# Optimization experiments

Hardware: AMD Instinct MI355X
Metric: run time of the kernel (lower is better)

The kernel has to match this reference:

```python
import jax, jax.numpy as jnp
import numpy as np

N = 50000
E = 800000
IN_C = 256
OUT_C = 128
HID = 2 * OUT_C  # 256


def setup_inputs() -> dict:
    key = jax.random.key(0)
    ks = jax.random.split(key, 8)
    def glorot(k, fan_in, fan_out):
        lim = (6.0 / (fan_in + fan_out)) ** 0.5
        return jax.random.uniform(k, (fan_in, fan_out), jnp.float32, -lim, lim)
    x = jax.random.normal(ks[0], (N, IN_C), dtype=jnp.float32)
    edge_index = jax.random.randint(ks[1], (2, E), 0, N, dtype=jnp.int64)
    return {
        "x": x,
        "edge_index": edge_index,
        "W1": glorot(ks[2], IN_C, HID),
        "b1": jnp.zeros((HID,), jnp.float32),
        "W_mu": glorot(ks[3], HID, OUT_C),
        "b_mu": jnp.zeros((OUT_C,), jnp.float32),
        "W_ls": glorot(ks[4], HID, OUT_C),
        "b_ls": jnp.zeros((OUT_C,), jnp.float32),
    }


def _gcn_norm(edge_index, n):
    # PyG GCNConv default: add self-loops, symmetric normalization D^-1/2 A D^-1/2
    loop = jnp.arange(n, dtype=edge_index.dtype)
    src = jnp.concatenate([edge_index[0], loop])  # [E+N]
    dst = jnp.concatenate([edge_index[1], loop])
    deg = jax.ops.segment_sum(jnp.ones_like(dst, dtype=jnp.float32), dst, num_segments=n)
    dinv = jnp.where(deg > 0, jax.lax.rsqrt(deg), 0.0)
    norm = dinv[src] * dinv[dst]  # [E+N]
    return src, dst, norm


def _gcn_conv(x, W, b, src, dst, norm, n):
    h = x @ W                                   # [N, F_out] transform first (F_out < F_in ok)
    msg = h[src] * norm[:, None]                # [E+N, F_out] gather + scale
    out = jax.ops.segment_sum(msg, dst, num_segments=n)  # scatter-add aggregate
    return out + b


def reference(x, edge_index, W1, b1, W_mu, b_mu, W_ls, b_ls):
    n = x.shape[0]
    src, dst, norm = _gcn_norm(edge_index, n)
    h = jax.nn.relu(_gcn_conv(x, W1, b1, src, dst, norm, n))
    mu = _gcn_conv(h, W_mu, b_mu, src, dst, norm, n)
    logstd = _gcn_conv(h, W_ls, b_ls, src, dst, norm, n)
    return (mu, logstd)
```

## Files before the change

kernel.cpp:

```cpp
#include <hip/hip_runtime.h>

#define NN 50000
#define EE 800000
#define NBIN 196
#define BINCAP 4608
#define NB_P1 391
#define NB_PA 6250
#define NB_PB 256

typedef _Float16 half8 __attribute__((ext_vector_type(8)));
typedef float f32x4 __attribute__((ext_vector_type(4)));
typedef unsigned short ushort8v __attribute__((ext_vector_type(8)));
typedef unsigned short ushort4v __attribute__((ext_vector_type(4)));

__device__ __forceinline__ unsigned short f2h(float f){
  _Float16 h = (_Float16)f; unsigned short u; __builtin_memcpy(&u, &h, 2); return u;
}
__device__ __forceinline__ float h2f(unsigned short u){
  _Float16 h; __builtin_memcpy(&h, &u, 2); return (float)h;
}
__device__ __forceinline__ void split2h(float v, unsigned short* p){
  _Float16 hi = (_Float16)v;
  _Float16 lo = (_Float16)(v - (float)hi);
  __builtin_memcpy(p, &hi, 2);
  __builtin_memcpy(p+1, &lo, 2);
}
__device__ __forceinline__ void gl2lds16(const unsigned short* g, unsigned short* l){
  __builtin_amdgcn_global_load_lds(
    (const __attribute__((address_space(1))) unsigned int*)g,
    (__attribute__((address_space(3))) unsigned int*)l, 16, 0, 0);
}

__device__ __forceinline__ int detect_m(const int* eidx, int* sh){
  int t = threadIdx.x;
  if (t < 64){
    int v = eidx[2*t + 1];
    unsigned long long nz = __ballot(v != 0);
    if (t == 0) *sh = (nz == 0ULL) ? 1 : 0;
  }
  __syncthreads();
  return *sh;
}

__global__ __launch_bounds__(512) void k_prep(const int* __restrict__ eidx,
    const float* __restrict__ X, const float* __restrict__ W1,
    const float* __restrict__ Wmu, const float* __restrict__ Wls,
    int* __restrict__ gcur, unsigned int* __restrict__ binbuf,
    unsigned short* __restrict__ Asp, unsigned short* __restrict__ Bt1,
    unsigned short* __restrict__ Bt2){
  int b = blockIdx.x;
  int tid = threadIdx.x;
  if (b < NB_P1){
    __shared__ int msh;
    __shared__ int hist[NBIN];
    __shared__ int base[NBIN];
    int m = detect_m(eidx, &msh);
    for (int k = tid; k < NBIN; k += 512) hist[k] = 0;
    __syncthreads();
    int sv[4], dl[4], cb[4], ofs[4];
    #pragma unroll
    for (int j = 0; j < 4; ++j){
      int e = b*2048 + j*512 + tid;
      cb[j] = -1;
      if (e < EE){
        sv[j] = m ? eidx[2*e]        : eidx[e];
        int d  = m ? eidx[2*(EE + e)] : eidx[EE + e];
        cb[j] = d >> 8; dl[j] = d & 255;
        ofs[j] = atomicAdd(&hist[cb[j]], 1);
      }
    }
    __syncthreads();
    for (int k = tid; k < NBIN; k += 512)
      base[k] = hist[k] ? atomicAdd(&gcur[k], hist[k]) : 0;
    __syncthreads();
    #pragma unroll
    for (int j = 0; j < 4; ++j){
      if (cb[j] >= 0){
        int p = base[cb[j]] + ofs[j];
        if (p < BINCAP)
          binbuf[(size_t)cb[j]*BINCAP + p] = (unsigned)sv[j] | ((unsigned)dl[j] << 16);
      }
    }
  } else if (b < NB_P1 + NB_PA){
    int gid = (b - NB_P1)*512 + tid;
    int r = gid >> 6, t = gid & 63;
    float4 v = *(const float4*)(X + (size_t)r*256 + t*4);
    __attribute__((aligned(16))) unsigned short sh[8];
    split2h(v.x, sh); split2h(v.y, sh+2); split2h(v.z, sh+4); split2h(v.w, sh+6);
    *(uint4*)(Asp + (size_t)r*512 + t*8) = *(const uint4*)(sh);
  } else {
    int gid = (b - NB_P1 - NB_PA)*512 + tid;
    int idx = gid & 65535;
    int n = idx & 255, k = idx >> 8;
    if (gid < 65536){
      unsigned short hq = f2h(W1[k*256 + n]);
      unsigned short* p = Bt1 + (size_t)n*512 + 2*k;
      p[0] = hq; p[1] = hq;
    } else {
      float w = (n < 128) ? Wmu[k*128 + n] : Wls[k*128 + (n - 128)];
      Bt2[(size_t)n*256 + k] = f2h(w);
    }
  }
}

__global__ __launch_bounds__(512) void k_pass2(const unsigned int* __restrict__ binbuf,
    const int* __restrict__ gcur, int* __restrict__ cnt,
    unsigned short* __restrict__ bk){
  __shared__ int lcnt[256];
  __shared__ __align__(16) unsigned short lbk[256*64];
  int c = blockIdx.x;
  int tid = threadIdx.x;
  if (tid < 256) lcnt[tid] = 0;
  __syncthreads();
  int n = gcur[c]; if (n > BINCAP) n = BINCAP;
  const unsigned int* bb = binbuf + (size_t)c*BINCAP;
  for (int t = tid; t < n; t += 512){
    unsigned v = bb[t];
    int dloc = v >> 16;
    int slot = atomicAdd(&lcnt[dloc], 1);
    if (slot < 64) lbk[dloc*64 + slot] = (unsigned short)(v & 0xFFFF);
  }
  __syncthreads();
  #pragma unroll
  for (int k = 0; k < 4; ++k){
    int idx = k*512 + tid;
    int node = c*256 + (idx >> 3);
    if (node < NN)
      *(uint4*)(bk + (size_t)c*256*64 + idx*8) = *(const uint4*)(lbk + idx*8);
  }
  if (tid < 256){
    int node = c*256 + tid;
    if (node < NN) cnt[node] = lcnt[tid];
  }
}

template<int KT, int SCALE>
__global__ __launch_bounds__(256) void k_gemm(const unsigned short* __restrict__ Asp,
                                              const unsigned short* __restrict__ Bt,
                                              unsigned short* __restrict__ C, int M,
                                              const int* __restrict__ cnt){
  __shared__ __align__(16) unsigned short sA[128*64];
  __shared__ __align__(16) unsigned short sB[128*64];
  const int tid  = threadIdx.x;
  const int wave = tid >> 6, lane = tid & 63;
  const int wm = wave >> 1, wn = wave & 1;
  const int quad = lane >> 4, l16 = lane & 15;
  const int tM = blockIdx.x, tN = blockIdx.y;
  const int rsub = lane >> 3;
  const int chs  = (lane & 7) ^ rsub;

  f32x4 acc[4][4] = {};

  for (int kt = 0; kt < KT; ++kt){
    #pragma unroll
    for (int j = 0; j < 4; ++j){
      int q = wave*4 + j;
      int r = q*8 + rsub;
      int arow = tM*128 + r; if (arow >= M) arow = M-1;
      gl2lds16(Asp + (size_t)arow*(KT*64) + kt*64 + chs*8, &sA[q*512]);
      gl2lds16(Bt  + (size_t)(tN*128 + r)*(KT*64) + kt*64 + chs*8, &sB[q*512]);
    }
    __syncthreads();
    #pragma unroll
    for (int ks = 0; ks < 2; ++ks){
      half8 af[4], bfr[4];
      #pragma unroll
      for (int t = 0; t < 4; ++t){
        int R = wm*64 + t*16 + l16;
        af[t]  = *(const half8*)(&sA[R*64 + ((ks*4 + quad) ^ (R & 7))*8]);
      }
      #pragma unroll
      for (int t = 0; t < 4; ++t){
        int R = wn*64 + t*16 + l16;
        bfr[t] = *(const half8*)(&sB[R*64 + ((ks*4 + quad) ^ (R & 7))*8]);
      }
      #pragma unroll
      for (int mt = 0; mt < 4; ++mt)
        #pragma unroll
        for (int nt = 0; nt < 4; ++nt)
          acc[mt][nt] = __builtin_amdgcn_mfma_f32_16x16x32_f16(af[mt], bfr[nt], acc[mt][nt], 0, 0, 0);
    }
    __syncthreads();
  }

  #pragma unroll
  for (int mt = 0; mt < 4; ++mt){
    #pragma unroll
    for (int r = 0; r < 4; ++r){
      int row = tM*128 + wm*64 + mt*16 + quad*4 + r;
      if (row < M){
        float sc = 1.f;
        if (SCALE) sc = rsqrtf((float)(cnt[row] + 1));
        #pragma unroll
        for (int nt = 0; nt < 4; ++nt){
          int cc = tN*128 + wn*64 + nt*16 + l16;
          C[(size_t)row*256 + cc] = f2h(acc[mt][nt][r] * sc);
        }
      }
    }
  }
}

__global__ __launch_bounds__(256) void k_agg_relu(const unsigned short* __restrict__ feat,
    const int* __restrict__ cnt, const unsigned short* __restrict__ bkall,
    const float* __restrict__ b1, unsigned short* __restrict__ h1){
  int i = blockIdx.x*4 + (threadIdx.x >> 6);
  int lane = threadIdx.x & 63;
  int f0 = lane*4;
  int deg = cnt[i]; if (deg > 64) deg = 64;
  float di = rsqrtf((float)(deg + 1));
  const unsigned short* bk = bkall + ((size_t)i << 6);
  ushort4 hv = *(const ushort4*)(feat + (size_t)i*256 + f0);
  float p0 = h2f(hv.x), p1 = h2f(hv.y), p2 = h2f(hv.z), p3 = h2f(hv.w);
  float q0=0.f,q1=0.f,q2=0.f,q3=0.f, r0=0.f,r1=0.f,r2=0.f,r3=0.f, t0=0.f,t1=0.f,t2=0.f,t3=0.f;
  int e = 0;
  for (; e + 8 <= deg; e += 8){
    ushort8v sa = *(const ushort8v*)(bk + e);
    ushort4 v0 = *(const ushort4*)(feat + (size_t)sa[0]*256 + f0);
    ushort4 v1 = *(const ushort4*)(feat + (size_t)sa[1]*256 + f0);
    ushort4 v2 = *(const ushort4*)(feat + (size_t)sa[2]*256 + f0);
    ushort4 v3 = *(const ushort4*)(feat + (size_t)sa[3]*256 + f0);
    ushort4 v4 = *(const ushort4*)(feat + (size_t)sa[4]*256 + f0);
    ushort4 v5 = *(const ushort4*)(feat + (size_t)sa[5]*256 + f0);
    ushort4 v6 = *(const ushort4*)(feat + (size_t)sa[6]*256 + f0);
    ushort4 v7 = *(const ushort4*)(feat + (size_t)sa[7]*256 + f0);
    p0 += h2f(v0.x); p1 += h2f(v0.y); p2 += h2f(v0.z); p3 += h2f(v0.w);
    q0 += h2f(v1.x); q1 += h2f(v1.y); q2 += h2f(v1.z); q3 += h2f(v1.w);
    r0 += h2f(v2.x); r1 += h2f(v2.y); r2 += h2f(v2.z); r3 += h2f(v2.w);
    t0 += h2f(v3.x); t1 += h2f(v3.y); t2 += h2f(v3.z); t3 += h2f(v3.w);
    p0 += h2f(v4.x); p1 += h2f(v4.y); p2 += h2f(v4.z); p3 += h2f(v4.w);
    q0 += h2f(v5.x); q1 += h2f(v5.y); q2 += h2f(v5.z); q3 += h2f(v5.w);
    r0 += h2f(v6.x); r1 += h2f(v6.y); r2 += h2f(v6.z); r3 += h2f(v6.w);
    t0 += h2f(v7.x); t1 += h2f(v7.y); t2 += h2f(v7.z); t3 += h2f(v7.w);
  }
  if (e + 4 <= deg){
    ushort4v sa = *(const ushort4v*)(bk + e);
    ushort4 v0 = *(const ushort4*)(feat + (size_t)sa[0]*256 + f0);
    ushort4 v1 = *(const ushort4*)(feat + (size_t)sa[1]*256 + f0);
    ushort4 v2 = *(const ushort4*)(feat + (size_t)sa[2]*256 + f0);
    ushort4 v3 = *(const ushort4*)(feat + (size_t)sa[3]*256 + f0);
    p0 += h2f(v0.x); p1 += h2f(v0.y); p2 += h2f(v0.z); p3 += h2f(v0.w);
    q0 += h2f(v1.x); q1 += h2f(v1.y); q2 += h2f(v1.z); q3 += h2f(v1.w);
    r0 += h2f(v2.x); r1 += h2f(v2.y); r2 += h2f(v2.z); r3 += h2f(v2.w);
    t0 += h2f(v3.x); t1 += h2f(v3.y); t2 += h2f(v3.z); t3 += h2f(v3.w);
    e += 4;
  }
  for (; e < deg; ++e){
    int s = bk[e];
    ushort4 v = *(const ushort4*)(feat + (size_t)s*256 + f0);
    p0 += h2f(v.x); p1 += h2f(v.y); p2 += h2f(v.z); p3 += h2f(v.w);
  }
  float s0 = p0+q0+r0+t0, s1 = p1+q1+r1+t1, s2 = p2+q2+r2+t2, s3 = p3+q3+r3+t3;
  float4 bb = *(const float4*)(b1 + f0);
  float u0 = fmaxf(di*s0 + bb.x, 0.f);
  float u1 = fmaxf(di*s1 + bb.y, 0.f);
  float u2 = fmaxf(di*s2 + bb.z, 0.f);
  float u3 = fmaxf(di*s3 + bb.w, 0.f);
  ushort4 o;
  o.x = f2h(di*u0); o.y = f2h(di*u1); o.z = f2h(di*u2); o.w = f2h(di*u3);
  *(ushort4*)(h1 + (size_t)i*256 + f0) = o;
}

__global__ __launch_bounds__(256) void k_agg_out(const unsigned short* __restrict__ feat,
    const int* __restrict__ cnt, const unsigned short* __restrict__ bkall,
    const float* __restrict__ bmu, const float* __restrict__ bls, float* __restrict__ outp){
  int i = blockIdx.x*4 + (threadIdx.x >> 6);
  int lane = threadIdx.x & 63;
  int f0 = lane*4;
  int deg = cnt[i]; if (deg > 64) deg = 64;
  float di = rsqrtf((float)(deg + 1));
  const unsigned short* bk = bkall + ((size_t)i << 6);
  ushort4 hv = *(const ushort4*)(feat + (size_t)i*256 + f0);
  float p0 = h2f(hv.x), p1 = h2f(hv.y), p2 = h2f(hv.z), p3 = h2f(hv.w);
  float q0=0.f,q1=0.f,q2=0.f,q3=0.f, r0=0.f,r1=0.f,r2=0.f,r3=0.f, t0=0.f,t1=0.f,t2=0.f,t3=0.f;
  int e = 0;
  for (; e + 8 <= deg; e += 8){
    ushort8v sa = *(const ushort8v*)(bk + e);
    ushort4 v0 = *(const ushort4*)(feat + (size_t)sa[0]*256 + f0);
    ushort4 v1 = *(const ushort4*)(feat + (size_t)sa[1]*256 + f0);
    ushort4 v2 = *(const ushort4*)(feat + (size_t)sa[2]*256 + f0);
    ushort4 v3 = *(const ushort4*)(feat + (size_t)sa[3]*256 + f0);
    ushort4 v4 = *(const ushort4*)(feat + (size_t)sa[4]*256 + f0);
    ushort4 v5 = *(const ushort4*)(feat + (size_t)sa[5]*256 + f0);
    ushort4 v6 = *(const ushort4*)(feat + (size_t)sa[6]*256 + f0);
    ushort4 v7 = *(const ushort4*)(feat + (size_t)sa[7]*256 + f0);
    p0 += h2f(v0.x); p1 += h2f(v0.y); p2 += h2f(v0.z); p3 += h2f(v0.w);
    q0 += h2f(v1.x); q1 += h2f(v1.y); q2 += h2f(v1.z); q3 += h2f(v1.w);
    r0 += h2f(v2.x); r1 += h2f(v2.y); r2 += h2f(v2.z); r3 += h2f(v2.w);
    t0 += h2f(v3.x); t1 += h2f(v3.y); t2 += h2f(v3.z); t3 += h2f(v3.w);
    p0 += h2f(v4.x); p1 += h2f(v4.y); p2 += h2f(v4.z); p3 += h2f(v4.w);
    q0 += h2f(v5.x); q1 += h2f(v5.y); q2 += h2f(v5.z); q3 += h2f(v5.w);
    r0 += h2f(v6.x); r1 += h2f(v6.y); r2 += h2f(v6.z); r3 += h2f(v6.w);
    t0 += h2f(v7.x); t1 += h2f(v7.y); t2 += h2f(v7.z); t3 += h2f(v7.w);
  }
  if (e + 4 <= deg){
    ushort4v sa = *(const ushort4v*)(bk + e);
    ushort4 v0 = *(const ushort4*)(feat + (size_t)sa[0]*256 + f0);
    ushort4 v1 = *(const ushort4*)(feat + (size_t)sa[1]*256 + f0);
    ushort4 v2 = *(const ushort4*)(feat + (size_t)sa[2]*256 + f0);
    ushort4 v3 = *(const ushort4*)(feat + (size_t)sa[3]*256 + f0);
    p0 += h2f(v0.x); p1 += h2f(v0.y); p2 += h2f(v0.z); p3 += h2f(v0.w);
    q0 += h2f(v1.x); q1 += h2f(v1.y); q2 += h2f(v1.z); q3 += h2f(v1.w);
    r0 += h2f(v2.x); r1 += h2f(v2.y); r2 += h2f(v2.z); r3 += h2f(v2.w);
    t0 += h2f(v3.x); t1 += h2f(v3.y); t2 += h2f(v3.z); t3 += h2f(v3.w);
    e += 4;
  }
  for (; e < deg; ++e){
    int s = bk[e];
    ushort4 v = *(const ushort4*)(feat + (size_t)s*256 + f0);
    p0 += h2f(v.x); p1 += h2f(v.y); p2 += h2f(v.z); p3 += h2f(v.w);
  }
  float a0 = di*(p0+q0+r0+t0), a1 = di*(p1+q1+r1+t1);
  float a2 = di*(p2+q2+r2+t2), a3 = di*(p3+q3+r3+t3);
  float4 o;
  if (f0 < 128){
    float4 bb = *(const float4*)(bmu + f0);
    o.x = a0 + bb.x; o.y = a1 + bb.y; o.z = a2 + bb.z; o.w = a3 + bb.w;
    *(float4*)(outp + (size_t)i*128 + f0) = o;
  } else {
    int g = f0 - 128;
    float4 bb = *(const float4*)(bls + g);
    o.x = a0 + bb.x; o.y = a1 + bb.y; o.z = a2 + bb.z; o.w = a3 + bb.w;
    *(float4*)(outp + (size_t)NN*128 + (size_t)i*128 + g) = o;
  }
}

extern "C" void kernel_launch(void* const* d_in, const int* in_sizes, int n_in,
                              void* d_out, int out_size, void* d_ws, size_t ws_size,
                              hipStream_t stream){
  const float* x   = (const float*)d_in[0];
  const int* eidx  = (const int*)d_in[1];
  const float* W1  = (const float*)d_in[2];
  const float* b1  = (const float*)d_in[3];
  const float* Wmu = (const float*)d_in[4];
  const float* bmu = (const float*)d_in[5];
  const float* Wls = (const float*)d_in[6];
  const float* bls = (const float*)d_in[7];
  float* out = (float*)d_out;

  char* ws = (char*)d_ws;
  size_t off = 0;
  auto alloc = [&](size_t bytes)->char*{
    char* p = ws + off; off = (off + bytes + 511) & ~(size_t)511; return p;
  };
  int* gcur     = (int*)alloc(NBIN*4);
  unsigned int* binbuf = (unsigned int*)alloc((size_t)NBIN*BINCAP*4);
  int* cnt      = (int*)alloc(NN*4);
  unsigned short* buckets = (unsigned short*)alloc((size_t)NN*64*2);
  unsigned short* Bt1 = (unsigned short*)alloc((size_t)256*512*2);
  unsigned short* Bt2 = (unsigned short*)alloc((size_t)256*256*2);
  unsigned short* AspX = (unsigned short*)alloc((size_t)NN*512*2);
  unsigned short* h1  = (unsigned short*)alloc((size_t)NN*256*2);
  unsigned short* h   = (unsigned short*)alloc((size_t)NN*256*2);
  unsigned short* z   = h;

  hipMemsetAsync(gcur, 0, NBIN*4, stream);
  k_prep<<<NB_P1 + NB_PA + NB_PB, 512, 0, stream>>>(eidx, x, W1, Wmu, Wls,
                                                    gcur, binbuf, AspX, Bt1, Bt2);
  k_pass2<<<NBIN, 512, 0, stream>>>(binbuf, gcur, cnt, buckets);
  k_gemm<8,1><<<dim3(391, 2), 256, 0, stream>>>(AspX, Bt1, h, NN, cnt);
  k_agg_relu<<<12500, 256, 0, stream>>>(h, cnt, buckets, b1, h1);
  k_gemm<4,0><<<dim3(391, 2), 256, 0, stream>>>(h1, Bt2, z, NN, cnt);
  k_agg_out<<<12500, 256, 0, stream>>>(z, cnt, buckets, bmu, bls, out);
}
```

Before: 297.0 us.

## Use 16-byte gathers with half-wave per node and software-pipelined neighbor loads

The two aggregation kernels now give each node 32 lanes that each own 8 features, so every neighbour row is fetched with 16-byte loads instead of 8-byte loads, and each block covers 8 nodes. The gather loop is software-pipelined so the next batch of 8 neighbour rows is in flight while the current batch is summed. The aim is fewer memory instructions and more memory-level parallelism in these latency-bound gathers. The cost is more registers held per thread, which may reduce occupancy.

```diff
diff --git a/kernel.cpp b/kernel.cpp
--- a/kernel.cpp
+++ b/kernel.cpp
@@ -201,127 +201,135 @@
   }
 }
 
+struct B8 { ushort8v r0,r1,r2,r3,r4,r5,r6,r7; };
+
+__device__ __forceinline__ void load_b8(B8& d, const unsigned short* __restrict__ feat,
+                                        ushort8v ix, int f0){
+  d.r0 = *(const ushort8v*)(feat + (size_t)ix[0]*256 + f0);
+  d.r1 = *(const ushort8v*)(feat + (size_t)ix[1]*256 + f0);
+  d.r2 = *(const ushort8v*)(feat + (size_t)ix[2]*256 + f0);
+  d.r3 = *(const ushort8v*)(feat + (size_t)ix[3]*256 + f0);
+  d.r4 = *(const ushort8v*)(feat + (size_t)ix[4]*256 + f0);
+  d.r5 = *(const ushort8v*)(feat + (size_t)ix[5]*256 + f0);
+  d.r6 = *(const ushort8v*)(feat + (size_t)ix[6]*256 + f0);
+  d.r7 = *(const ushort8v*)(feat + (size_t)ix[7]*256 + f0);
+}
+__device__ __forceinline__ void acc_b8(const B8& s, float* pa, float* pb){
+  #pragma unroll
+  for (int k = 0; k < 8; ++k) pa[k] += h2f(s.r0[k]);
+  #pragma unroll
+  for (int k = 0; k < 8; ++k) pb[k] += h2f(s.r1[k]);
+  #pragma unroll
+  for (int k = 0; k < 8; ++k) pa[k] += h2f(s.r2[k]);
+  #pragma unroll
+  for (int k = 0; k < 8; ++k) pb[k] += h2f(s.r3[k]);
+  #pragma unroll
+  for (int k = 0; k < 8; ++k) pa[k] += h2f(s.r4[k]);
+  #pragma unroll
+  for (int k = 0; k < 8; ++k) pb[k] += h2f(s.r5[k]);
+  #pragma unroll
+  for (int k = 0; k < 8; ++k) pa[k] += h2f(s.r6[k]);
+  #pragma unroll
+  for (int k = 0; k < 8; ++k) pb[k] += h2f(s.r7[k]);
+}
+
+__device__ __forceinline__ void gather_sum(const unsigned short* __restrict__ feat,
+    const unsigned short* __restrict__ bk, int i, int deg, int f0,
+    float* pa, float* pb){
+  ushort8v hv = *(const ushort8v*)(feat + (size_t)i*256 + f0);
+  #pragma unroll
+  for (int k = 0; k < 8; ++k){ pa[k] = h2f(hv[k]); pb[k] = 0.f; }
+  int nb = deg >> 3;
+  int e = nb << 3;
+  if (nb > 0){
+    ushort8v ixA = *(const ushort8v*)(bk);
+    B8 bA; load_b8(bA, feat, ixA, f0);
+    for (int t = 1; t < nb; ++t){
+      ushort8v ixB = *(const ushort8v*)(bk + t*8);
+      B8 bB; load_b8(bB, feat, ixB, f0);
+      acc_b8(bA, pa, pb);
+      bA = bB;
+    }
+    acc_b8(bA, pa, pb);
+  }
+  if (e + 4 <= deg){
+    ushort4v ix = *(const ushort4v*)(bk + e);
+    ushort8v v0 = *(const ushort8v*)(feat + (size_t)ix[0]*256 + f0);
+    ushort8v v1 = *(const ushort8v*)(feat + (size_t)ix[1]*256 + f0);
+    ushort8v v2 = *(const ushort8v*)(feat + (size_t)ix[2]*256 + f0);
+    ushort8v v3 = *(const ushort8v*)(feat + (size_t)ix[3]*256 + f0);
+    #pragma unroll
+    for (int k = 0; k < 8; ++k) pa[k] += h2f(v0[k]);
+    #pragma unroll
+    for (int k = 0; k < 8; ++k) pb[k] += h2f(v1[k]);
+    #pragma unroll
+    for (int k = 0; k < 8; ++k) pa[k] += h2f(v2[k]);
+    #pragma unroll
+    for (int k = 0; k < 8; ++k) pb[k] += h2f(v3[k]);
+    e += 4;
+  }
+  for (; e < deg; ++e){
+    int s = bk[e];
+    ushort8v v = *(const ushort8v*)(feat + (size_t)s*256 + f0);
+    #pragma unroll
+    for (int k = 0; k < 8; ++k) pa[k] += h2f(v[k]);
+  }
+}
+
 __global__ __launch_bounds__(256) void k_agg_relu(const unsigned short* __restrict__ feat,
     const int* __restrict__ cnt, const unsigned short* __restrict__ bkall,
     const float* __restrict__ b1, unsigned short* __restrict__ h1){
-  int i = blockIdx.x*4 + (threadIdx.x >> 6);
-  int lane = threadIdx.x & 63;
-  int f0 = lane*4;
+  int i = blockIdx.x*8 + (threadIdx.x >> 5);
+  int lane = threadIdx.x & 31;
+  int f0 = lane*8;
   int deg = cnt[i]; if (deg > 64) deg = 64;
   float di = rsqrtf((float)(deg + 1));
   const unsigned short* bk = bkall + ((size_t)i << 6);
-  ushort4 hv = *(const ushort4*)(feat + (size_t)i*256 + f0);
-  float p0 = h2f(hv.x), p1 = h2f(hv.y), p2 = h2f(hv.z), p3 = h2f(hv.w);
-  float q0=0.f,q1=0.f,q2=0.f,q3=0.f, r0=0.f,r1=0.f,r2=0.f,r3=0.f, t0=0.f,t1=0.f,t2=0.f,t3=0.f;
-  int e = 0;
-  for (; e + 8 <= deg; e += 8){
-    ushort8v sa = *(const ushort8v*)(bk + e);
-    ushort4 v0 = *(const ushort4*)(feat + (size_t)sa[0]*256 + f0);
-    ushort4 v1 = *(const ushort4*)(feat + (size_t)sa[1]*256 + f0);
-    ushort4 v2 = *(const ushort4*)(feat + (size_t)sa[2]*256 + f0);
-    ushort4 v3 = *(const ushort4*)(feat + (size_t)sa[3]*256 + f0);
-    ushort4 v4 = *(const ushort4*)(feat + (size_t)sa[4]*256 + f0);
-    ushort4 v5 = *(const ushort4*)(feat + (size_t)sa[5]*256 + f0);
-    ushort4 v6 = *(const ushort4*)(feat + (size_t)sa[6]*256 + f0);
-    ushort4 v7 = *(const ushort4*)(feat + (size_t)sa[7]*256 + f0);
-    p0 += h2f(v0.x); p1 += h2f(v0.y); p2 += h2f(v0.z); p3 += h2f(v0.w);
-    q0 += h2f(v1.x); q1 += h2f(v1.y); q2 += h2f(v1.z); q3 += h2f(v1.w);
-    r0 += h2f(v2.x); r1 += h2f(v2.y); r2 += h2f(v2.z); r3 += h2f(v2.w);
-    t0 += h2f(v3.x); t1 += h2f(v3.y); t2 += h2f(v3.z); t3 += h2f(v3.w);
-    p0 += h2f(v4.x); p1 += h2f(v4.y); p2 += h2f(v4.z); p3 += h2f(v4.w);
-    q0 += h2f(v5.x); q1 += h2f(v5.y); q2 += h2f(v5.z); q3 += h2f(v5.w);
-    r0 += h2f(v6.x); r1 += h2f(v6.y); r2 += h2f(v6.z); r3 += h2f(v6.w);
-    t0 += h2f(v7.x); t1 += h2f(v7.y); t2 += h2f(v7.z); t3 += h2f(v7.w);
-  }
-  if (e + 4 <= deg){
-    ushort4v sa = *(const ushort4v*)(bk + e);
-    ushort4 v0 = *(const ushort4*)(feat + (size_t)sa[0]*256 + f0);
-    ushort4 v1 = *(const ushort4*)(feat + (size_t)sa[1]*256 + f0);
-    ushort4 v2 = *(const ushort4*)(feat + (size_t)sa[2]*256 + f0);
-    ushort4 v3 = *(const ushort4*)(feat + (size_t)sa[3]*256 + f0);
-    p0 += h2f(v0.x); p1 += h2f(v0.y); p2 += h2f(v0.z); p3 += h2f(v0.w);
-    q0 += h2f(v1.x); q1 += h2f(v1.y); q2 += h2f(v1.z); q3 += h2f(v1.w);
-    r0 += h2f(v2.x); r1 += h2f(v2.y); r2 += h2f(v2.z); r3 += h2f(v2.w);
-    t0 += h2f(v3.x); t1 += h2f(v3.y); t2 += h2f(v3.z); t3 += h2f(v3.w);
-    e += 4;
-  }
-  for (; e < deg; ++e){
-    int s = bk[e];
-    ushort4 v = *(const ushort4*)(feat + (size_t)s*256 + f0);
-    p0 += h2f(v.x); p1 += h2f(v.y); p2 += h2f(v.z); p3 += h2f(v.w);
-  }
-  float s0 = p0+q0+r0+t0, s1 = p1+q1+r1+t1, s2 = p2+q2+r2+t2, s3 = p3+q3+r3+t3;
-  float4 bb = *(const float4*)(b1 + f0);
-  float u0 = fmaxf(di*s0 + bb.x, 0.f);
-  float u1 = fmaxf(di*s1 + bb.y, 0.f);
-  float u2 = fmaxf(di*s2 + bb.z, 0.f);
-  float u3 = fmaxf(di*s3 + bb.w, 0.f);
-  ushort4 o;
-  o.x = f2h(di*u0); o.y = f2h(di*u1); o.z = f2h(di*u2); o.w = f2h(di*u3);
-  *(ushort4*)(h1 + (size_t)i*256 + f0) = o;
+  float pa[8], pb[8];
+  gather_sum(feat, bk, i, deg, f0, pa, pb);
+  float4 bb0 = *(const float4*)(b1 + f0);
+  float4 bb1 = *(const float4*)(b1 + f0 + 4);
+  float bbv[8] = {bb0.x, bb0.y, bb0.z, bb0.w, bb1.x, bb1.y, bb1.z, bb1.w};
+  ushort8v o;
+  #pragma unroll
+  for (int k = 0; k < 8; ++k){
+    float u = fmaxf(di*(pa[k] + pb[k]) + bbv[k], 0.f);
+    o[k] = f2h(di*u);
+  }
+  *(ushort8v*)(h1 + (size_t)i*256 + f0) = o;
 }
 
 __global__ __launch_bounds__(256) void k_agg_out(const unsigned short* __restrict__ feat,
     const int* __restrict__ cnt, const unsigned short* __restrict__ bkall,
     const float* __restrict__ bmu, const float* __restrict__ bls, float* __restrict__ outp){
-  int i = blockIdx.x*4 + (threadIdx.x >> 6);
-  int lane = threadIdx.x & 63;
-  int f0 = lane*4;
+  int i = blockIdx.x*8 + (threadIdx.x >> 5);
+  int lane = threadIdx.x & 31;
+  int f0 = lane*8;
   int deg = cnt[i]; if (deg > 64) deg = 64;
   float di = rsqrtf((float)(deg + 1));
   const unsigned short* bk = bkall + ((size_t)i << 6);
-  ushort4 hv = *(const ushort4*)(feat + (size_t)i*256 + f0);
-  float p0 = h2f(hv.x), p1 = h2f(hv.y), p2 = h2f(hv.z), p3 = h2f(hv.w);
-  float q0=0.f,q1=0.f,q2=0.f,q3=0.f, r0=0.f,r1=0.f,r2=0.f,r3=0.f, t0=0.f,t1=0.f,t2=0.f,t3=0.f;
-  int e = 0;
-  for (; e + 8 <= deg; e += 8){
-    ushort8v sa = *(const ushort8v*)(bk + e);
-    ushort4 v0 = *(const ushort4*)(feat + (size_t)sa[0]*256 + f0);
-    ushort4 v1 = *(const ushort4*)(feat + (size_t)sa[1]*256 + f0);
-    ushort4 v2 = *(const ushort4*)(feat + (size_t)sa[2]*256 + f0);
-    ushort4 v3 = *(const ushort4*)(feat + (size_t)sa[3]*256 + f0);
-    ushort4 v4 = *(const ushort4*)(feat + (size_t)sa[4]*256 + f0);
-    ushort4 v5 = *(const ushort4*)(feat + (size_t)sa[5]*256 + f0);
-    ushort4 v6 = *(const ushort4*)(feat + (size_t)sa[6]*256 + f0);
-    ushort4 v7 = *(const ushort4*)(feat + (size_t)sa[7]*256 + f0);
-    p0 += h2f(v0.x); p1 += h2f(v0.y); p2 += h2f(v0.z); p3 += h2f(v0.w);
-    q0 += h2f(v1.x); q1 += h2f(v1.y); q2 += h2f(v1.z); q3 += h2f(v1.w);
-    r0 += h2f(v2.x); r1 += h2f(v2.y); r2 += h2f(v2.z); r3 += h2f(v2.w);
-    t0 += h2f(v3.x); t1 += h2f(v3.y); t2 += h2f(v3.z); t3 += h2f(v3.w);
-    p0 += h2f(v4.x); p1 += h2f(v4.y); p2 += h2f(v4.z); p3 += h2f(v4.w);
-    q0 += h2f(v5.x); q1 += h2f(v5.y); q2 += h2f(v5.z); q3 += h2f(v5.w);
-    r0 += h2f(v6.x); r1 += h2f(v6.y); r2 += h2f(v6.z); r3 += h2f(v6.w);
-    t0 += h2f(v7.x); t1 += h2f(v7.y); t2 += h2f(v7.z); t3 += h2f(v7.w);
-  }
-  if (e + 4 <= deg){
-    ushort4v sa = *(const ushort4v*)(bk + e);
-    ushort4 v0 = *(const ushort4*)(feat + (size_t)sa[0]*256 + f0);
-    ushort4 v1 = *(const ushort4*)(feat + (size_t)sa[1]*256 + f0);
-    ushort4 v2 = *(const ushort4*)(feat + (size_t)sa[2]*256 + f0);
-    ushort4 v3 = *(const ushort4*)(feat + (size_t)sa[3]*256 + f0);
-    p0 += h2f(v0.x); p1 += h2f(v0.y); p2 += h2f(v0.z); p3 += h2f(v0.w);
-    q0 += h2f(v1.x); q1 += h2f(v1.y); q2 += h2f(v1.z); q3 += h2f(v1.w);
-    r0 += h2f(v2.x); r1 += h2f(v2.y); r2 += h2f(v2.z); r3 += h2f(v2.w);
-    t0 += h2f(v3.x); t1 += h2f(v3.y); t2 += h2f(v3.z); t3 += h2f(v3.w);
-    e += 4;
-  }
-  for (; e < deg; ++e){
-    int s = bk[e];
-    ushort4 v = *(const ushort4*)(feat + (size_t)s*256 + f0);
-    p0 += h2f(v.x); p1 += h2f(v.y); p2 += h2f(v.z); p3 += h2f(v.w);
-  }
-  float a0 = di*(p0+q0+r0+t0), a1 = di*(p1+q1+r1+t1);
-  float a2 = di*(p2+q2+r2+t2), a3 = di*(p3+q3+r3+t3);
-  float4 o;
+  float pa[8], pb[8];
+  gather_sum(feat, bk, i, deg, f0, pa, pb);
+  float a[8];
+  #pragma unroll
+  for (int k = 0; k < 8; ++k) a[k] = di*(pa[k] + pb[k]);
   if (f0 < 128){
-    float4 bb = *(const float4*)(bmu + f0);
-    o.x = a0 + bb.x; o.y = a1 + bb.y; o.z = a2 + bb.z; o.w = a3 + bb.w;
-    *(float4*)(outp + (size_t)i*128 + f0) = o;
+    float4 bb0 = *(const float4*)(bmu + f0);
+    float4 bb1 = *(const float4*)(bmu + f0 + 4);
+    float4 o0, o1;
+    o0.x = a[0]+bb0.x; o0.y = a[1]+bb0.y; o0.z = a[2]+bb0.z; o0.w = a[3]+bb0.w;
+    o1.x = a[4]+bb1.x; o1.y = a[5]+bb1.y; o1.z = a[6]+bb1.z; o1.w = a[7]+bb1.w;
+    *(float4*)(outp + (size_t)i*128 + f0) = o0;
+    *(float4*)(outp + (size_t)i*128 + f0 + 4) = o1;
   } else {
     int g = f0 - 128;
-    float4 bb = *(const float4*)(bls + g);
-    o.x = a0 + bb.x; o.y = a1 + bb.y; o.z = a2 + bb.z; o.w = a3 + bb.w;
-    *(float4*)(outp + (size_t)NN*128 + (size_t)i*128 + g) = o;
+    float4 bb0 = *(const float4*)(bls + g);
+    float4 bb1 = *(const float4*)(bls + g + 4);
+    float4 o0, o1;
+    o0.x = a[0]+bb0.x; o0.y = a[1]+bb0.y; o0.z = a[2]+bb0.z; o0.w = a[3]+bb0.w;
+    o1.x = a[4]+bb1.x; o1.y = a[5]+bb1.y; o1.z = a[6]+bb1.z; o1.w = a[7]+bb1.w;
+    *(float4*)(outp + (size_t)NN*128 + (size_t)i*128 + g) = o0;
+    *(float4*)(outp + (size_t)NN*128 + (size_t)i*128 + g + 4) = o1;
   }
 }
 
@@ -359,7 +367,7 @@
                                                     gcur, binbuf, AspX, Bt1, Bt2);
   k_pass2<<<NBIN, 512, 0, stream>>>(binbuf, gcur, cnt, buckets);
   k_gemm<8,1><<<dim3(391, 2), 256, 0, stream>>>(AspX, Bt1, h, NN, cnt);
-  k_agg_relu<<<12500, 256, 0, stream>>>(h, cnt, buckets, b1, h1);
+  k_agg_relu<<<6250, 256, 0, stream>>>(h, cnt, buckets, b1, h1);
   k_gemm<4,0><<<dim3(391, 2), 256, 0, stream>>>(h1, Bt2, z, NN, cnt);
-  k_agg_out<<<12500, 256, 0, stream>>>(z, cnt, buckets, bmu, bls, out);
-}
+  k_agg_out<<<6250, 256, 0, stream>>>(z, cnt, buckets, bmu, bls, out);
+}
```

New measurement: 301.2 us. About the same (+1.4%).

## Fuse layer-1 aggregation with second GEMM via per-block MFMA; halve bucket size

Applied to the files above, without the earlier changes.

The first-layer aggregation+ReLU kernel now also performs the second-layer GEMM. Each 1024-thread block aggregates 16 nodes into a swizzled LDS tile, and each wave computes a 16-column slice with MFMA 16x16x32 f16 against Bt2 before writing z. This removes the h1 round trip through global memory and one kernel launch. The binning also switches to 128-node bins (391 bins, smaller capacity) so k_pass2 runs more blocks with less LDS. In exchange, Bt2 is reloaded from global/L2 per block, and the fused kernel carries extra syncthreads and a large block size, which may lower occupancy.

```diff
diff --git a/kernel.cpp b/kernel.cpp
--- a/kernel.cpp
+++ b/kernel.cpp
@@ -2,8 +2,8 @@
 
 #define NN 50000
 #define EE 800000
-#define NBIN 196
-#define BINCAP 4608
+#define NBIN 391
+#define BINCAP 2560
 #define NB_P1 391
 #define NB_PA 6250
 #define NB_PB 256
@@ -65,7 +65,7 @@
       if (e < EE){
         sv[j] = m ? eidx[2*e]        : eidx[e];
         int d  = m ? eidx[2*(EE + e)] : eidx[EE + e];
-        cb[j] = d >> 8; dl[j] = d & 255;
+        cb[j] = d >> 7; dl[j] = d & 127;
         ofs[j] = atomicAdd(&hist[cb[j]], 1);
       }
     }
@@ -106,11 +106,11 @@
 __global__ __launch_bounds__(512) void k_pass2(const unsigned int* __restrict__ binbuf,
     const int* __restrict__ gcur, int* __restrict__ cnt,
     unsigned short* __restrict__ bk){
-  __shared__ int lcnt[256];
-  __shared__ __align__(16) unsigned short lbk[256*64];
+  __shared__ int lcnt[128];
+  __shared__ __align__(16) unsigned short lbk[128*64];
   int c = blockIdx.x;
   int tid = threadIdx.x;
-  if (tid < 256) lcnt[tid] = 0;
+  if (tid < 128) lcnt[tid] = 0;
   __syncthreads();
   int n = gcur[c]; if (n > BINCAP) n = BINCAP;
   const unsigned int* bb = binbuf + (size_t)c*BINCAP;
@@ -122,14 +122,14 @@
   }
   __syncthreads();
   #pragma unroll
-  for (int k = 0; k < 4; ++k){
+  for (int k = 0; k < 2; ++k){
     int idx = k*512 + tid;
-    int node = c*256 + (idx >> 3);
+    int node = c*128 + (idx >> 3);
     if (node < NN)
-      *(uint4*)(bk + (size_t)c*256*64 + idx*8) = *(const uint4*)(lbk + idx*8);
-  }
-  if (tid < 256){
-    int node = c*256 + tid;
+      *(uint4*)(bk + (size_t)c*128*64 + idx*8) = *(const uint4*)(lbk + idx*8);
+  }
+  if (tid < 128){
+    int node = c*128 + tid;
     if (node < NN) cnt[node] = lcnt[tid];
   }
 }
@@ -201,11 +201,15 @@
   }
 }
 
-__global__ __launch_bounds__(256) void k_agg_relu(const unsigned short* __restrict__ feat,
+__global__ __launch_bounds__(1024) void k_agg_gemm(const unsigned short* __restrict__ feat,
     const int* __restrict__ cnt, const unsigned short* __restrict__ bkall,
-    const float* __restrict__ b1, unsigned short* __restrict__ h1){
-  int i = blockIdx.x*4 + (threadIdx.x >> 6);
-  int lane = threadIdx.x & 63;
+    const float* __restrict__ b1, const unsigned short* __restrict__ Bt2,
+    unsigned short* __restrict__ z){
+  __shared__ __align__(16) unsigned short hT[16*256];
+  int tid = threadIdx.x;
+  int nl = tid >> 6;
+  int i = blockIdx.x*16 + nl;
+  int lane = tid & 63;
   int f0 = lane*4;
   int deg = cnt[i]; if (deg > 64) deg = 64;
   float di = rsqrtf((float)(deg + 1));
@@ -252,13 +256,35 @@
   }
   float s0 = p0+q0+r0+t0, s1 = p1+q1+r1+t1, s2 = p2+q2+r2+t2, s3 = p3+q3+r3+t3;
   float4 bb = *(const float4*)(b1 + f0);
-  float u0 = fmaxf(di*s0 + bb.x, 0.f);
-  float u1 = fmaxf(di*s1 + bb.y, 0.f);
-  float u2 = fmaxf(di*s2 + bb.z, 0.f);
-  float u3 = fmaxf(di*s3 + bb.w, 0.f);
   ushort4 o;
-  o.x = f2h(di*u0); o.y = f2h(di*u1); o.z = f2h(di*u2); o.w = f2h(di*u3);
-  *(ushort4*)(h1 + (size_t)i*256 + f0) = o;
+  o.x = f2h(di*fmaxf(di*s0 + bb.x, 0.f));
+  o.y = f2h(di*fmaxf(di*s1 + bb.y, 0.f));
+  o.z = f2h(di*fmaxf(di*s2 + bb.z, 0.f));
+  o.w = f2h(di*fmaxf(di*s3 + bb.w, 0.f));
+  {
+    int chunk = lane >> 1;
+    int sw = ((chunk ^ (nl & 7)) << 3) + ((lane & 1) << 2);
+    *(ushort4*)(&hT[nl*256 + sw]) = o;
+  }
+  __syncthreads();
+  const int l16 = lane & 15, quad = lane >> 4;
+  f32x4 acc = {};
+  #pragma unroll
+  for (int kk = 0; kk < 8; ++kk){
+    half8 af = *(const half8*)(&hT[l16*256 + (((kk*4 + quad) ^ (l16 & 7)) << 3)]);
+    half8 bf = *(const half8*)(Bt2 + (size_t)(nl*16 + l16)*256 + kk*32 + quad*8);
+    acc = __builtin_amdgcn_mfma_f32_16x16x32_f16(af, bf, acc, 0, 0, 0);
+  }
+  __syncthreads();
+  #pragma unroll
+  for (int r = 0; r < 4; ++r)
+    hT[(quad*4 + r)*256 + nl*16 + l16] = f2h(acc[r]);
+  __syncthreads();
+  {
+    int nw = tid >> 6, g0 = (tid & 63)*4;
+    *(ushort4*)(z + (size_t)(blockIdx.x*16 + nw)*256 + g0) =
+        *(const ushort4*)(&hT[nw*256 + g0]);
+  }
 }
 
 __global__ __launch_bounds__(256) void k_agg_out(const unsigned short* __restrict__ feat,
@@ -350,16 +376,15 @@
   unsigned short* Bt1 = (unsigned short*)alloc((size_t)256*512*2);
   unsigned short* Bt2 = (unsigned short*)alloc((size_t)256*256*2);
   unsigned short* AspX = (unsigned short*)alloc((size_t)NN*512*2);
-  unsigned short* h1  = (unsigned short*)alloc((size_t)NN*256*2);
   unsigned short* h   = (unsigned short*)alloc((size_t)NN*256*2);
   unsigned short* z   = h;
+  unsigned short* zbuf = (unsigned short*)alloc((size_t)NN*256*2);
 
   hipMemsetAsync(gcur, 0, NBIN*4, stream);
   k_prep<<<NB_P1 + NB_PA + NB_PB, 512, 0, stream>>>(eidx, x, W1, Wmu, Wls,
                                                     gcur, binbuf, AspX, Bt1, Bt2);
   k_pass2<<<NBIN, 512, 0, stream>>>(binbuf, gcur, cnt, buckets);
   k_gemm<8,1><<<dim3(391, 2), 256, 0, stream>>>(AspX, Bt1, h, NN, cnt);
-  k_agg_relu<<<12500, 256, 0, stream>>>(h, cnt, buckets, b1, h1);
-  k_gemm<4,0><<<dim3(391, 2), 256, 0, stream>>>(h1, Bt2, z, NN, cnt);
-  k_agg_out<<<12500, 256, 0, stream>>>(z, cnt, buckets, bmu, bls, out);
-}
+  k_agg_gemm<<<3125, 1024, 0, stream>>>(h, cnt, buckets, b1, Bt2, zbuf);
+  k_agg_out<<<12500, 256, 0, stream>>>(zbuf, cnt, buckets, bmu, bls, out);
+}
```

New measurement: 349.7 us. +17.7%, slower.
